# Performance work log

Hardware: AMD Instinct MI355X
Metric: run time of the kernel (lower is better)

The kernel has to match this reference:

```python
import jax, jax.numpy as jnp
import numpy as np

B, S, HID = 1, 2048, 2048
H, NOPE, ROPE, VDIM = 16, 128, 64, 128
QR, KVR = 1536, 512
IH, ID = 16, 128
TOPK = 512
THETA = 10000.0
EPS = 1e-6
SCALE = (NOPE + ROPE) ** -0.5
NEG = -1e9


def _cos_sin(s, dim, dtype):
    inv = 1.0 / (THETA ** (np.arange(0, dim, 2, dtype=np.float32) / dim))
    t = np.arange(s, dtype=np.float32)
    f = np.outer(t, inv)
    emb = np.concatenate([f, f], -1)
    return jnp.asarray(np.cos(emb), dtype), jnp.asarray(np.sin(emb), dtype)


def _rope(x, cos, sin):
    # x: [b,s,h,d]; cos/sin: [s,d]; NeoX-style rotate_half
    x1, x2 = jnp.split(x, 2, axis=-1)
    rot = jnp.concatenate([-x2, x1], axis=-1)
    return x * cos[None, :, None, :] + rot * sin[None, :, None, :]


def _rmsnorm(x, w):
    v = jnp.mean(x.astype(jnp.float32) ** 2, -1, keepdims=True)
    return (x.astype(jnp.float32) * jax.lax.rsqrt(v + EPS)).astype(x.dtype) * w


def _layernorm(x, w, b):
    m = jnp.mean(x, -1, keepdims=True)
    v = jnp.var(x, -1, keepdims=True)
    return (x - m) * jax.lax.rsqrt(v + EPS) * w + b


def setup_inputs() -> dict:
    key = jax.random.key(0)
    ks = jax.random.split(key, 12)
    g = lambda k, shp: jax.random.normal(k, shp, jnp.float32) * 0.02
    return {
        'hidden_states': jax.random.normal(ks[0], (B, S, HID), jnp.float32),
        'q_a_w': g(ks[1], (QR, HID)),
        'q_a_ln_w': jnp.ones((QR,), jnp.float32),
        'q_b_w': g(ks[2], (H * (NOPE + ROPE), QR)),
        'kv_a_w': g(ks[3], (KVR + ROPE, HID)),
        'kv_a_ln_w': jnp.ones((KVR,), jnp.float32),
        'kv_b_w': g(ks[4], (H * (NOPE + VDIM), KVR)),
        'o_w': g(ks[5], (HID, H * VDIM)),
        'idx_wq_b_w': g(ks[6], (IH * ID, QR)),
        'idx_wk_w': g(ks[7], (ID, HID)),
        'idx_kn_w': jnp.ones((ID,), jnp.float32),
        'idx_kn_b': jnp.zeros((ID,), jnp.float32),
        'idx_wproj_w': g(ks[8], (IH, HID)),
    }


def reference(hidden_states, q_a_w, q_a_ln_w, q_b_w, kv_a_w, kv_a_ln_w, kv_b_w, o_w,
              idx_wq_b_w, idx_wk_w, idx_kn_w, idx_kn_b, idx_wproj_w):
    b, s, _ = hidden_states.shape
    cos, sin = _cos_sin(s, ROPE, hidden_states.dtype)

    # --- MLA projections ---
    qr = _rmsnorm(hidden_states @ q_a_w.T, q_a_ln_w)                 # [b,s,QR]
    q = (qr @ q_b_w.T).reshape(b, s, H, NOPE + ROPE)
    q_nope, q_pe = q[..., :NOPE], q[..., NOPE:]
    q_pe = _rope(q_pe, cos, sin)
    ckv = hidden_states @ kv_a_w.T                                   # [b,s,KVR+ROPE]
    c_kv, k_pe = ckv[..., :KVR], ckv[..., KVR:]
    k_pe = _rope(k_pe[:, :, None, :], cos, sin)                      # [b,s,1,ROPE]
    kv = (_rmsnorm(c_kv, kv_a_ln_w) @ kv_b_w.T).reshape(b, s, H, NOPE + VDIM)
    k_nope, v = kv[..., :NOPE], kv[..., NOPE:]

    # --- DSA indexer: per-token importance scores ---
    iq = (qr @ idx_wq_b_w.T).reshape(b, s, IH, ID)
    iq = jnp.concatenate([_rope(iq[..., :ROPE], cos, sin), iq[..., ROPE:]], -1)
    ik = _layernorm(hidden_states @ idx_wk_w.T, idx_kn_w, idx_kn_b)  # [b,s,ID]
    ik_pe = _rope(ik[:, :, None, :ROPE], cos, sin)[:, :, 0, :]
    ik = jnp.concatenate([ik_pe, ik[..., ROPE:]], -1)
    iw = (hidden_states @ idx_wproj_w.T) * (IH ** -0.5)              # [b,s,IH]
    idx_scores = jnp.einsum('bqh,bhqk->bqk', iw,
                            jax.nn.relu(jnp.einsum('bqhd,bkd->bhqk', iq, ik)))
    causal = jnp.tril(jnp.ones((s, s), bool))
    idx_scores = jnp.where(causal[None], idx_scores, -jnp.inf)
    _, top_idx = jax.lax.top_k(idx_scores, TOPK)                     # [b,s,TOPK]
    bi = jnp.arange(b)[:, None, None]
    qi = jnp.arange(s)[None, :, None]
    keep = jnp.zeros((b, s, s), bool).at[bi, qi, top_idx].set(True)
    allowed = keep & causal[None]                                    # [b,s,s]

    # --- sparse top-k attention (top-k mask to -inf before softmax) ---
    qh = jnp.concatenate([q_nope, q_pe], -1)                         # [b,s,H,192]
    kh = jnp.concatenate([k_nope, jnp.broadcast_to(k_pe, (b, s, H, ROPE))], -1)
    scores = jnp.einsum('bqhd,bkhd->bhqk', qh, kh) * SCALE
    scores = jnp.where(allowed[:, None], scores, NEG)
    attn = jax.nn.softmax(scores, -1)
    out = jnp.einsum('bhqk,bkhd->bqhd', attn, v).reshape(b, s, H * VDIM)
    return out @ o_w.T
```

## Files before the change

kernel.cpp:

```cpp
#include <hip/hip_runtime.h>
#include <hip/hip_bf16.h>
#include <math.h>

#define SEQ 2048
#define HIDD 2048
#define QRANK 1536
#define KVRANK 512
#define TOPK 512
#define EPSF 1e-6f
#define SCALE_ATTN 0.07216878364870323f
#define NCAT 1680

typedef __attribute__((ext_vector_type(8))) short short8v;
typedef __attribute__((ext_vector_type(4))) short short4v;
typedef __attribute__((ext_vector_type(4))) float f32x4;

__device__ inline unsigned short f2bf(float f) {
    unsigned u = __float_as_uint(f);
    unsigned r = (u + 0x7FFFu + ((u >> 16) & 1u)) >> 16;
    return (unsigned short)r;
}
__device__ inline float bf2f(unsigned short b) {
    return __uint_as_float(((unsigned)b) << 16);
}
__device__ inline void split2(float x, unsigned short& h, unsigned short& l) {
    h = f2bf(x);
    l = f2bf(x - bf2f(h));
}

__device__ inline short4v ds_read_tr16(const void* p) {
#if __has_builtin(__builtin_amdgcn_ds_read_tr16_b64)
    return __builtin_amdgcn_ds_read_tr16_b64((short4v*)p);
#else
    const unsigned short* u = (const unsigned short*)p;
    short4v r;
    r[0] = (short)u[0]; r[1] = (short)u[16]; r[2] = (short)u[32]; r[3] = (short)u[48];
    return r;
#endif
}

__global__ __launch_bounds__(256) void cvt_bf16_4_kernel(
    const float* __restrict__ a, int na4, const float* __restrict__ b, int nb4,
    const float* __restrict__ c, int nc4, const float* __restrict__ d, int nd4,
    unsigned short* __restrict__ oa, unsigned short* __restrict__ ob,
    unsigned short* __restrict__ oc, unsigned short* __restrict__ od,
    float* __restrict__ cos_t, float* __restrict__ sin_t)
{
    if (blockIdx.x < SEQ && threadIdx.x < 32) {
        int s = blockIdx.x, i = threadIdx.x;
        double inv = pow(10000.0, -((double)(2 * i)) / 64.0);
        double f = (double)s * inv;
        cos_t[s * 32 + i] = (float)cos(f);
        sin_t[s * 32 + i] = (float)sin(f);
    }
    int total = na4 + nb4 + nc4 + nd4;
    for (int i = blockIdx.x * 256 + threadIdx.x; i < total; i += gridDim.x * 256) {
        const float* src; unsigned short* dst; int j = i;
        if (j < na4) { src = a; dst = oa; }
        else if ((j -= na4) < nb4) { src = b; dst = ob; }
        else if ((j -= nb4) < nc4) { src = c; dst = oc; }
        else { j -= nc4; src = d; dst = od; }
        float4 v = ((const float4*)src)[j];
        ushort4 o;
        o.x = f2bf(v.x); o.y = f2bf(v.y); o.z = f2bf(v.z); o.w = f2bf(v.w);
        ((ushort4*)dst)[j] = o;
    }
}

__global__ __launch_bounds__(256) void cvt_split3_kernel(
    const float* __restrict__ hidden, const float* __restrict__ q_a_w,
    const float* __restrict__ idx_wk_w, const float* __restrict__ idx_wproj_w,
    const float* __restrict__ wq,
    unsigned short* __restrict__ hidh, unsigned short* __restrict__ hidl,
    unsigned short* __restrict__ catwh, unsigned short* __restrict__ catwl,
    unsigned short* __restrict__ wqh, unsigned short* __restrict__ wql)
{
    const int nhid4 = HIDD * HIDD / 4;
    const int ncat4 = NCAT * HIDD / 4;
    const int nwq4  = HIDD * QRANK / 4;
    int total = nhid4 + ncat4 + nwq4;
    for (int i = blockIdx.x * 256 + threadIdx.x; i < total; i += gridDim.x * 256) {
        int j = i;
        const float4* s4;
        unsigned short *dh, *dl;
        float scale = 1.f;
        if (j < nhid4) {
            s4 = (const float4*)hidden + j; dh = hidh; dl = hidl;
        } else if ((j -= nhid4) < ncat4) {
            int row = (j * 4) >> 11;
            dh = catwh; dl = catwl;
            if (row < 1536) s4 = (const float4*)q_a_w + j;
            else if (row < 1664) s4 = (const float4*)idx_wk_w + (j - 1536 * 512);
            else { s4 = (const float4*)idx_wproj_w + (j - 1664 * 512); scale = 0.25f; }
        } else {
            j -= ncat4;
            s4 = (const float4*)wq + j; dh = wqh; dl = wql;
        }
        float4 v = *s4;
        float xs[4] = {v.x * scale, v.y * scale, v.z * scale, v.w * scale};
        ushort4 oh, ol;
        unsigned short h2, l2;
        split2(xs[0], h2, l2); oh.x = h2; ol.x = l2;
        split2(xs[1], h2, l2); oh.y = h2; ol.y = l2;
        split2(xs[2], h2, l2); oh.z = h2; ol.z = l2;
        split2(xs[3], h2, l2); oh.w = h2; ol.w = l2;
        ((ushort4*)dh)[j] = oh;
        ((ushort4*)dl)[j] = ol;
    }
}

__global__ __launch_bounds__(256) void wkt_kernel(const float* __restrict__ kvb,
                                                  unsigned short* __restrict__ wkt) {
    __shared__ float t[128][129];
    int h = blockIdx.x, n0 = blockIdx.y * 128;
    int tid = threadIdx.x;
    for (int it = tid; it < 128 * 32; it += 256) {
        int d = it >> 5, c4 = it & 31;
        float4 v = *(const float4*)(kvb + ((size_t)(h * 256 + d)) * 512 + n0 + c4 * 4);
        t[d][c4 * 4 + 0] = v.x; t[d][c4 * 4 + 1] = v.y;
        t[d][c4 * 4 + 2] = v.z; t[d][c4 * 4 + 3] = v.w;
    }
    __syncthreads();
    for (int it = tid; it < 128 * 32; it += 256) {
        int n = it >> 5, dc = it & 31;
        ushort4 o;
        o.x = f2bf(t[dc * 4 + 0][n]); o.y = f2bf(t[dc * 4 + 1][n]);
        o.z = f2bf(t[dc * 4 + 2][n]); o.w = f2bf(t[dc * 4 + 3][n]);
        *(ushort4*)(wkt + ((size_t)h * 512 + n0 + n) * 128 + dc * 4) = o;
    }
}

__global__ __launch_bounds__(256) void gemm_cat_split_kernel(
    const float* __restrict__ hidden, const float* __restrict__ q_a_w,
    const float* __restrict__ idx_wk_w, const float* __restrict__ idx_wproj_w,
    const unsigned short* __restrict__ hidh, const unsigned short* __restrict__ hidl,
    const unsigned short* __restrict__ catwh, const unsigned short* __restrict__ catwl,
    float* __restrict__ ccat)
{
    __shared__ __align__(16) unsigned short Ah[128 * 32], Al[128 * 32];
    __shared__ __align__(16) unsigned short Bh[128 * 32], Bl[128 * 32];
    int tid = threadIdx.x;
    int l = tid & 63, w = tid >> 6;
    int wr = w >> 1, wc = w & 1;
    int m0 = blockIdx.x * 128, n0 = blockIdx.y * 128;
    const bool pre = (hidh != nullptr);
    f32x4 acc[4][4] = {};
    for (int k0 = 0; k0 < HIDD; k0 += 32) {
        __syncthreads();
#pragma unroll
        for (int i = 0; i < 2; ++i) {
            int idx = tid + i * 256;
            int r = idx >> 2, cc = idx & 3;
            int sw = cc ^ (r & 3);
            int gb = n0 + r; if (gb > NCAT - 1) gb = NCAT - 1;
            if (pre) {
                size_t abase = (size_t)(m0 + r) * HIDD + k0 + cc * 8;
                *(short8v*)&Ah[r * 32 + sw * 8] = *(const short8v*)(hidh + abase);
                *(short8v*)&Al[r * 32 + sw * 8] = *(const short8v*)(hidl + abase);
                size_t bbase = (size_t)gb * HIDD + k0 + cc * 8;
                *(short8v*)&Bh[r * 32 + sw * 8] = *(const short8v*)(catwh + bbase);
                *(short8v*)&Bl[r * 32 + sw * 8] = *(const short8v*)(catwl + bbase);
            } else {
                {
                    const float* src = hidden + (size_t)(m0 + r) * HIDD + k0 + cc * 8;
                    float4 f0 = *(const float4*)src, f1 = *(const float4*)(src + 4);
                    float xs[8] = {f0.x, f0.y, f0.z, f0.w, f1.x, f1.y, f1.z, f1.w};
                    short8v dh, dl;
#pragma unroll
                    for (int e = 0; e < 8; ++e) {
                        unsigned short hh, ll; split2(xs[e], hh, ll);
                        dh[e] = (short)hh; dl[e] = (short)ll;
                    }
                    *(short8v*)&Ah[r * 32 + sw * 8] = dh;
                    *(short8v*)&Al[r * 32 + sw * 8] = dl;
                }
                {
                    float scale = 1.f;
                    const float* src;
                    if (gb < 1536) src = q_a_w + (size_t)gb * HIDD;
                    else if (gb < 1664) src = idx_wk_w + (size_t)(gb - 1536) * HIDD;
                    else { src = idx_wproj_w + (size_t)(gb - 1664) * HIDD; scale = 0.25f; }
                    src += k0 + cc * 8;
                    float4 f0 = *(const float4*)src, f1 = *(const float4*)(src + 4);
                    float xs[8] = {f0.x, f0.y, f0.z, f0.w, f1.x, f1.y, f1.z, f1.w};
                    short8v dh, dl;
#pragma unroll
                    for (int e = 0; e < 8; ++e) {
                        unsigned short hh, ll; split2(xs[e] * scale, hh, ll);
                        dh[e] = (short)hh; dl[e] = (short)ll;
                    }
                    *(short8v*)&Bh[r * 32 + sw * 8] = dh;
                    *(short8v*)&Bl[r * 32 + sw * 8] = dl;
                }
            }
        }
        __syncthreads();
        short8v avh[4], avl[4];
#pragma unroll
        for (int mt = 0; mt < 4; ++mt) {
            int row = wr * 64 + mt * 16 + (l & 15);
            int ch = (l >> 4) ^ (row & 3);
            avh[mt] = *(const short8v*)&Ah[row * 32 + ch * 8];
            avl[mt] = *(const short8v*)&Al[row * 32 + ch * 8];
        }
#pragma unroll
        for (int nt = 0; nt < 4; ++nt) {
            int row = wc * 64 + nt * 16 + (l & 15);
            int ch = (l >> 4) ^ (row & 3);
            short8v bvh = *(const short8v*)&Bh[row * 32 + ch * 8];
            short8v bvl = *(const short8v*)&Bl[row * 32 + ch * 8];
#pragma unroll
            for (int mt = 0; mt < 4; ++mt) {
                acc[mt][nt] = __builtin_amdgcn_mfma_f32_16x16x32_bf16(avh[mt], bvh, acc[mt][nt], 0, 0, 0);
                acc[mt][nt] = __builtin_amdgcn_mfma_f32_16x16x32_bf16(avh[mt], bvl, acc[mt][nt], 0, 0, 0);
                acc[mt][nt] = __builtin_amdgcn_mfma_f32_16x16x32_bf16(avl[mt], bvh, acc[mt][nt], 0, 0, 0);
            }
        }
    }
#pragma unroll
    for (int mt = 0; mt < 4; ++mt)
#pragma unroll
        for (int nt = 0; nt < 4; ++nt)
#pragma unroll
            for (int i = 0; i < 4; ++i) {
                int gm = m0 + wr * 64 + mt * 16 + (l >> 4) * 4 + i;
                int gn = n0 + wc * 64 + nt * 16 + (l & 15);
                if (gn < NCAT) ccat[(size_t)gm * NCAT + gn] = acc[mt][nt][i];
            }
}

__global__ __launch_bounds__(256) void gemm_iq_split_kernel(
    const float* __restrict__ qr, const float* __restrict__ wq,
    const unsigned short* __restrict__ qrh, const unsigned short* __restrict__ qrl,
    const unsigned short* __restrict__ wqh, const unsigned short* __restrict__ wql,
    const float* __restrict__ cos_t, const float* __restrict__ sin_t,
    unsigned short* __restrict__ iqh, unsigned short* __restrict__ iql)
{
    __shared__ __align__(16) unsigned short Ah[128 * 32], Al[128 * 32];
    __shared__ __align__(16) unsigned short Bh[128 * 32], Bl[128 * 32];
    int tid = threadIdx.x;
    int l = tid & 63, w = tid >> 6;
    int wr = w >> 1, wc = w & 1;
    int m0 = blockIdx.x * 128, n0 = blockIdx.y * 128;
    int hh_ = blockIdx.y;
    const bool pre = (wqh != nullptr);
    f32x4 acc[4][4] = {};
    for (int k0 = 0; k0 < QRANK; k0 += 32) {
        __syncthreads();
#pragma unroll
        for (int i = 0; i < 2; ++i) {
            int idx = tid + i * 256;
            int r = idx >> 2, cc = idx & 3;
            int sw = cc ^ (r & 3);
            if (pre) {
                size_t abase = (size_t)(m0 + r) * QRANK + k0 + cc * 8;
                *(short8v*)&Ah[r * 32 + sw * 8] = *(const short8v*)(qrh + abase);
                *(short8v*)&Al[r * 32 + sw * 8] = *(const short8v*)(qrl + abase);
                size_t bbase = (size_t)(n0 + r) * QRANK + k0 + cc * 8;
                *(short8v*)&Bh[r * 32 + sw * 8] = *(const short8v*)(wqh + bbase);
                *(short8v*)&Bl[r * 32 + sw * 8] = *(const short8v*)(wql + bbase);
            } else {
                {
                    const float* src = qr + (size_t)(m0 + r) * QRANK + k0 + cc * 8;
                    float4 f0 = *(const float4*)src, f1 = *(const float4*)(src + 4);
                    float xs[8] = {f0.x, f0.y, f0.z, f0.w, f1.x, f1.y, f1.z, f1.w};
                    short8v dh, dl;
#pragma unroll
                    for (int e = 0; e < 8; ++e) {
                        unsigned short h2, l2; split2(xs[e], h2, l2);
                        dh[e] = (short)h2; dl[e] = (short)l2;
                    }
                    *(short8v*)&Ah[r * 32 + sw * 8] = dh;
                    *(short8v*)&Al[r * 32 + sw * 8] = dl;
                }
                {
                    const float* src = wq + (size_t)(n0 + r) * QRANK + k0 + cc * 8;
                    float4 f0 = *(const float4*)src, f1 = *(const float4*)(src + 4);
                    float xs[8] = {f0.x, f0.y, f0.z, f0.w, f1.x, f1.y, f1.z, f1.w};
                    short8v dh, dl;
#pragma unroll
                    for (int e = 0; e < 8; ++e) {
                        unsigned short h2, l2; split2(xs[e], h2, l2);
                        dh[e] = (short)h2; dl[e] = (short)l2;
                    }
                    *(short8v*)&Bh[r * 32 + sw * 8] = dh;
                    *(short8v*)&Bl[r * 32 + sw * 8] = dl;
                }
            }
        }
        __syncthreads();
        short8v avh[4], avl[4];
#pragma unroll
        for (int mt = 0; mt < 4; ++mt) {
            int row = wr * 64 + mt * 16 + (l & 15);
            int ch = (l >> 4) ^ (row & 3);
            avh[mt] = *(const short8v*)&Ah[row * 32 + ch * 8];
            avl[mt] = *(const short8v*)&Al[row * 32 + ch * 8];
        }
#pragma unroll
        for (int nt = 0; nt < 4; ++nt) {
            int row = wc * 64 + nt * 16 + (l & 15);
            int ch = (l >> 4) ^ (row & 3);
            short8v bvh = *(const short8v*)&Bh[row * 32 + ch * 8];
            short8v bvl = *(const short8v*)&Bl[row * 32 + ch * 8];
#pragma unroll
            for (int mt = 0; mt < 4; ++mt) {
                acc[mt][nt] = __builtin_amdgcn_mfma_f32_16x16x32_bf16(avh[mt], bvh, acc[mt][nt], 0, 0, 0);
                acc[mt][nt] = __builtin_amdgcn_mfma_f32_16x16x32_bf16(avh[mt], bvl, acc[mt][nt], 0, 0, 0);
                acc[mt][nt] = __builtin_amdgcn_mfma_f32_16x16x32_bf16(avl[mt], bvh, acc[mt][nt], 0, 0, 0);
            }
        }
    }
    if (wc == 0) {
#pragma unroll
        for (int mt = 0; mt < 4; ++mt)
#pragma unroll
            for (int nt = 0; nt < 2; ++nt)
#pragma unroll
                for (int i = 0; i < 4; ++i) {
                    int q = m0 + wr * 64 + mt * 16 + (l >> 4) * 4 + i;
                    int dd = nt * 16 + (l & 15);
                    float c = cos_t[q * 32 + dd], s = sin_t[q * 32 + dd];
                    float x1 = acc[mt][nt][i], x2 = acc[mt][nt + 2][i];
                    acc[mt][nt][i] = x1 * c - x2 * s;
                    acc[mt][nt + 2][i] = x2 * c + x1 * s;
                }
    }
#pragma unroll
    for (int mt = 0; mt < 4; ++mt)
#pragma unroll
        for (int nt = 0; nt < 4; ++nt)
#pragma unroll
            for (int i = 0; i < 4; ++i) {
                int q = m0 + wr * 64 + mt * 16 + (l >> 4) * 4 + i;
                int d = wc * 64 + nt * 16 + (l & 15);
                size_t idx = ((size_t)q * 16 + hh_) * 128 + d;
                unsigned short h2, l2; split2(acc[mt][nt][i], h2, l2);
                iqh[idx] = h2; iql[idx] = l2;
            }
}

template <typename TA, typename TC>
__global__ __launch_bounds__(256) void mfma_nt_kernel(
    const TA* __restrict__ A, const unsigned short* __restrict__ B, TC* __restrict__ C,
    int M, int N, int K, int lda, int ldb, int ldc, long ab, long bb, long cb,
    const float* __restrict__ cos_t, const float* __restrict__ sin_t, int rope_mode)
{
    __shared__ __align__(16) unsigned short Asl[128 * 32];
    __shared__ __align__(16) unsigned short Bsl[128 * 32];
    int z = blockIdx.z;
    const TA* Az = A + (size_t)z * ab;
    const unsigned short* Bz = B + (size_t)z * bb;
    TC* Cz = C + (size_t)z * cb;
    int tid = threadIdx.x;
    int l = tid & 63, w = tid >> 6;
    int wr = w >> 1, wc = w & 1;
    int m0 = blockIdx.x * 128, n0 = blockIdx.y * 128;
    f32x4 acc[4][4] = {};

    for (int k0 = 0; k0 < K; k0 += 32) {
        __syncthreads();
#pragma unroll
        for (int i = 0; i < 2; ++i) {
            int idx = tid + i * 256;
            int r = idx >> 2, cc = idx & 3;
            int sw = cc ^ (r & 3);
            {
                short8v d;
                const TA* src = Az + (size_t)(m0 + r) * lda + k0 + cc * 8;
                if constexpr (sizeof(TA) == 2) {
                    d = *(const short8v*)src;
                } else {
                    float4 f0 = *(const float4*)src;
                    float4 f1 = *(const float4*)(src + 4);
                    d[0] = (short)f2bf(f0.x); d[1] = (short)f2bf(f0.y);
                    d[2] = (short)f2bf(f0.z); d[3] = (short)f2bf(f0.w);
                    d[4] = (short)f2bf(f1.x); d[5] = (short)f2bf(f1.y);
                    d[6] = (short)f2bf(f1.z); d[7] = (short)f2bf(f1.w);
                }
                *(short8v*)&Asl[r * 32 + sw * 8] = d;
            }
            {
                int gb = n0 + r; if (gb > N - 1) gb = N - 1;
                short8v d = *(const short8v*)(Bz + (size_t)gb * ldb + k0 + cc * 8);
                *(short8v*)&Bsl[r * 32 + sw * 8] = d;
            }
        }
        __syncthreads();
        short8v av[4], bv[4];
#pragma unroll
        for (int mt = 0; mt < 4; ++mt) {
            int row = wr * 64 + mt * 16 + (l & 15);
            int ch = (l >> 4) ^ (row & 3);
            av[mt] = *(const short8v*)&Asl[row * 32 + ch * 8];
        }
#pragma unroll
        for (int nt = 0; nt < 4; ++nt) {
            int row = wc * 64 + nt * 16 + (l & 15);
            int ch = (l >> 4) ^ (row & 3);
            bv[nt] = *(const short8v*)&Bsl[row * 32 + ch * 8];
        }
#pragma unroll
        for (int mt = 0; mt < 4; ++mt)
#pragma unroll
            for (int nt = 0; nt < 4; ++nt)
                acc[mt][nt] = __builtin_amdgcn_mfma_f32_16x16x32_bf16(av[mt], bv[nt], acc[mt][nt], 0, 0, 0);
    }
    if (rope_mode) {
        int gcol64 = (n0 >> 6) + wc;
        bool dorope = (rope_mode == 1) ? ((gcol64 % 3) == 2) : (gcol64 == 8);
        if (dorope) {
#pragma unroll
            for (int mt = 0; mt < 4; ++mt)
#pragma unroll
                for (int nt = 0; nt < 2; ++nt)
#pragma unroll
                    for (int i = 0; i < 4; ++i) {
                        int q = m0 + wr * 64 + mt * 16 + (l >> 4) * 4 + i;
                        int dd = nt * 16 + (l & 15);
                        float c = cos_t[q * 32 + dd], sn = sin_t[q * 32 + dd];
                        float x1 = acc[mt][nt][i], x2 = acc[mt][nt + 2][i];
                        acc[mt][nt][i] = x1 * c - x2 * sn;
                        acc[mt][nt + 2][i] = x2 * c + x1 * sn;
                    }
        }
    }
#pragma unroll
    for (int mt = 0; mt < 4; ++mt) {
#pragma unroll
        for (int nt = 0; nt < 4; ++nt) {
#pragma unroll
            for (int i = 0; i < 4; ++i) {
                int gm = m0 + wr * 64 + mt * 16 + (l >> 4) * 4 + i;
                int gn = n0 + wc * 64 + nt * 16 + (l & 15);
                if (gn < N) {
                    float v = acc[mt][nt][i];
                    if constexpr (sizeof(TC) == 4) Cz[(size_t)gm * ldc + gn] = v;
                    else Cz[(size_t)gm * ldc + gn] = f2bf(v);
                }
            }
        }
    }
}

__global__ __launch_bounds__(256) void rmsnorm_kernel(
    const float* __restrict__ in, const float* __restrict__ w, float* __restrict__ out,
    unsigned short* __restrict__ bf_out, unsigned short* __restrict__ bf_lo,
    int n, int in_stride)
{
    int row = blockIdx.x, tid = threadIdx.x;
    const float* x = in + (size_t)row * in_stride;
    float4 v[2];
    int cnt = 0;
    float ss = 0.f;
    int nf4 = n >> 2;
    for (int i = tid; i < nf4; i += 256) {
        float4 t = *(const float4*)(x + i * 4);
        v[cnt++] = t;
        ss += t.x * t.x + t.y * t.y + t.z * t.z + t.w * t.w;
    }
#pragma unroll
    for (int m = 32; m; m >>= 1) ss += __shfl_xor(ss, m);
    __shared__ float red[8];
    int wid = tid >> 6;
    if ((tid & 63) == 0) red[wid] = ss;
    __syncthreads();
    if (tid == 0) {
        float s = red[0] + red[1] + red[2] + red[3];
        red[4] = rsqrtf(s / (float)n + EPSF);
    }
    __syncthreads();
    float scale = red[4];
    cnt = 0;
    for (int i = tid; i < nf4; i += 256) {
        float4 t = v[cnt++];
        float4 wv = *(const float4*)(w + i * 4);
        float4 o;
        o.x = t.x * scale * wv.x; o.y = t.y * scale * wv.y;
        o.z = t.z * scale * wv.z; o.w = t.w * scale * wv.w;
        *(float4*)(out + (size_t)row * n + i * 4) = o;
        if (bf_out) {
            ushort4 ob;
            ob.x = f2bf(o.x); ob.y = f2bf(o.y); ob.z = f2bf(o.z); ob.w = f2bf(o.w);
            *(ushort4*)(bf_out + (size_t)row * n + i * 4) = ob;
            if (bf_lo) {
                ushort4 ol;
                ol.x = f2bf(o.x - bf2f(ob.x)); ol.y = f2bf(o.y - bf2f(ob.y));
                ol.z = f2bf(o.z - bf2f(ob.z)); ol.w = f2bf(o.w - bf2f(ob.w));
                *(ushort4*)(bf_lo + (size_t)row * n + i * 4) = ol;
            }
        }
    }
}

__global__ __launch_bounds__(256) void rmsnorm_khg_kernel(
    const float* __restrict__ ckv, const float* __restrict__ w,
    unsigned short* __restrict__ khg)
{
    int row = blockIdx.x, tid = threadIdx.x;
    const float* x = ckv + (size_t)row * 576;
    float4 v = make_float4(0.f, 0.f, 0.f, 0.f);
    float ss = 0.f;
    if (tid < 128) {
        v = *(const float4*)(x + tid * 4);
        ss = v.x * v.x + v.y * v.y + v.z * v.z + v.w * v.w;
    }
#pragma unroll
    for (int mm = 32; mm; mm >>= 1) ss += __shfl_xor(ss, mm);
    __shared__ float red[8];
    if ((tid & 63) == 0) red[tid >> 6] = ss;
    __syncthreads();
    if (tid == 0) red[4] = rsqrtf((red[0] + red[1] + red[2] + red[3]) * (1.f / 512.f) + EPSF);
    __syncthreads();
    float scale = red[4];
    if (tid < 128) {
        float4 wv = *(const float4*)(w + tid * 4);
        ushort4 ob;
        ob.x = f2bf(v.x * scale * wv.x); ob.y = f2bf(v.y * scale * wv.y);
        ob.z = f2bf(v.z * scale * wv.z); ob.w = f2bf(v.w * scale * wv.w);
        *(ushort4*)(khg + (size_t)row * 576 + tid * 4) = ob;
    } else if (tid < 192) {
        khg[(size_t)row * 576 + 512 + (tid - 128)] = f2bf(x[512 + tid - 128]);
    }
}

__global__ __launch_bounds__(64) void ln_rope_split_kernel(
    const float* __restrict__ in, int stride,
    const float* __restrict__ w, const float* __restrict__ b,
    const float* __restrict__ cos_t, const float* __restrict__ sin_t,
    unsigned short* __restrict__ ikh, unsigned short* __restrict__ ikl)
{
    int row = blockIdx.x, tid = threadIdx.x;
    const float* x = in + (size_t)row * stride;
    float x0 = x[tid], x1 = x[tid + 64];
    float s = x0 + x1, ss = x0 * x0 + x1 * x1;
#pragma unroll
    for (int m = 32; m; m >>= 1) { s += __shfl_xor(s, m); ss += __shfl_xor(ss, m); }
    float mean = s * (1.f / 128.f);
    float var = ss * (1.f / 128.f) - mean * mean;
    float r = rsqrtf(var + EPSF);
    float n0 = (x0 - mean) * r * w[tid] + b[tid];
    float n1 = (x1 - mean) * r * w[tid + 64] + b[tid + 64];
    float c = cos_t[row * 32 + (tid & 31)], sn = sin_t[row * 32 + (tid & 31)];
    float other = __shfl_xor(n0, 32);
    float r0 = (tid < 32) ? (n0 * c - other * sn) : (n0 * c + other * sn);
    unsigned short h2, l2;
    split2(r0, h2, l2);
    ikh[(size_t)row * 128 + tid] = h2; ikl[(size_t)row * 128 + tid] = l2;
    split2(n1, h2, l2);
    ikh[(size_t)row * 128 + 64 + tid] = h2; ikl[(size_t)row * 128 + 64 + tid] = l2;
}

__global__ __launch_bounds__(256) void idx_scores_mfma_kernel(
    const unsigned short* __restrict__ iqh, const unsigned short* __restrict__ iql,
    const unsigned short* __restrict__ ikh, const unsigned short* __restrict__ ikl,
    const float* __restrict__ iwsrc, int iw_stride,
    float* __restrict__ scores)
{
    int q0 = blockIdx.x * 64, k0 = blockIdx.y * 64;
    int tid = threadIdx.x;
    if (k0 > q0 + 63) {
        for (int t = tid; t < 64 * 64; t += 256) {
            int r = t >> 6, c = t & 63;
            scores[(size_t)(q0 + r) * SEQ + k0 + c] = -INFINITY;
        }
        return;
    }
    __shared__ __align__(16) unsigned short skh[64 * 128], skl[64 * 128];
    __shared__ __align__(16) unsigned short sqh[64 * 128], sql[64 * 128];
    __shared__ float iws[64][16];
    int l = tid & 63, w = tid >> 6;
    for (int it = tid; it < 64 * 16; it += 256) {
        int r = it >> 4, c = it & 15;
        int sw = c ^ (r & 15);
        *(short8v*)&skh[r * 128 + sw * 8] = *(const short8v*)(ikh + (size_t)(k0 + r) * 128 + c * 8);
        *(short8v*)&skl[r * 128 + sw * 8] = *(const short8v*)(ikl + (size_t)(k0 + r) * 128 + c * 8);
    }
    {
        int r = tid >> 2, c = tid & 3;
        *(float4*)&iws[r][c * 4] = *(const float4*)(iwsrc + (size_t)(q0 + r) * iw_stride + c * 4);
    }
    __syncthreads();
    short8v bhr[4][4], blr[4][4];
#pragma unroll
    for (int nt = 0; nt < 4; ++nt)
#pragma unroll
        for (int ks = 0; ks < 4; ++ks) {
            int brow = nt * 16 + (l & 15);
            int bch = ((l >> 4) + ks * 4) ^ (brow & 15);
            bhr[nt][ks] = *(const short8v*)&skh[brow * 128 + bch * 8];
            blr[nt][ks] = *(const short8v*)&skl[brow * 128 + bch * 8];
        }
    f32x4 acc[4] = {};
    for (int h = 0; h < 16; ++h) {
        __syncthreads();
        for (int it = tid; it < 64 * 16; it += 256) {
            int r = it >> 4, c = it & 15;
            int sw = c ^ (r & 15);
            size_t base = ((size_t)(q0 + r) * 16 + h) * 128 + c * 8;
            *(short8v*)&sqh[r * 128 + sw * 8] = *(const short8v*)(iqh + base);
            *(short8v*)&sql[r * 128 + sw * 8] = *(const short8v*)(iql + base);
        }
        __syncthreads();
        f32x4 dot[4] = {};
#pragma unroll
        for (int ks = 0; ks < 4; ++ks) {
            int arow = w * 16 + (l & 15);
            int ach = ((l >> 4) + ks * 4) ^ (arow & 15);
            short8v ah = *(const short8v*)&sqh[arow * 128 + ach * 8];
            short8v al = *(const short8v*)&sql[arow * 128 + ach * 8];
#pragma unroll
            for (int nt = 0; nt < 4; ++nt) {
                dot[nt] = __builtin_amdgcn_mfma_f32_16x16x32_bf16(ah, bhr[nt][ks], dot[nt], 0, 0, 0);
                dot[nt] = __builtin_amdgcn_mfma_f32_16x16x32_bf16(ah, blr[nt][ks], dot[nt], 0, 0, 0);
                dot[nt] = __builtin_amdgcn_mfma_f32_16x16x32_bf16(al, bhr[nt][ks], dot[nt], 0, 0, 0);
            }
        }
#pragma unroll
        for (int nt = 0; nt < 4; ++nt)
#pragma unroll
            for (int i = 0; i < 4; ++i) {
                float wv = iws[w * 16 + (l >> 4) * 4 + i][h];
                acc[nt][i] += wv * fmaxf(dot[nt][i], 0.f);
            }
    }
#pragma unroll
    for (int nt = 0; nt < 4; ++nt)
#pragma unroll
        for (int i = 0; i < 4; ++i) {
            int q = q0 + w * 16 + (l >> 4) * 4 + i;
            int k = k0 + nt * 16 + (l & 15);
            scores[(size_t)q * SEQ + k] = (k <= q) ? acc[nt][i] : -INFINITY;
        }
}

__global__ __launch_bounds__(1024) void topk_kernel(
    const float* __restrict__ scores, int* __restrict__ sel)
{
    int qi = blockIdx.x, tid = threadIdx.x;
    __shared__ unsigned long long keys[2048];
    const float* srow = scores + (size_t)qi * SEQ;
#pragma unroll
    for (int r = 0; r < 2; ++r) {
        int k = tid + r * 1024;
        unsigned u = __float_as_uint(srow[k]);
        unsigned mv = (u & 0x80000000u) ? ~u : (u | 0x80000000u);
        keys[k] = ((unsigned long long)mv << 32) | (unsigned)(2047 - k);
    }
    for (int ksz = 2; ksz <= 2048; ksz <<= 1) {
        for (int j = ksz >> 1; j > 0; j >>= 1) {
            __syncthreads();
#pragma unroll 1
            for (int r = 0; r < 2; ++r) {
                int i = tid + r * 1024;
                int ixj = i ^ j;
                if (ixj > i) {
                    unsigned long long a = keys[i], b = keys[ixj];
                    bool dir = ((i & ksz) == 0);
                    if ((a < b) == dir) { keys[i] = b; keys[ixj] = a; }
                }
            }
        }
    }
    __syncthreads();
    if (tid < TOPK) {
        int k = 2047 - (int)(keys[tid] & 0xFFFFFFFFu);
        sel[(size_t)qi * TOPK + tid] = (tid <= qi) ? k : -1;
    }
}

__global__ __launch_bounds__(256) void attn_mfma_kernel(
    const unsigned short* __restrict__ qabs,
    const float* __restrict__ qsrc,
    const unsigned short* __restrict__ khg,
    const int* __restrict__ sel,
    unsigned short* __restrict__ ocomp)
{
    __shared__ __align__(16) char smem[77312];
    unsigned short* plds = (unsigned short*)(smem + 74752);
    float* smax = (float*)(smem + 76800);
    float* ssum = (float*)(smem + 77056);

    const int qi = blockIdx.x;
    const int tid = threadIdx.x;
    const int l = tid & 63, w = tid >> 6;
    const int lg = l >> 4, lr = l & 15;
    const int nv = min(TOPK, qi + 1);
    const int ntile = (nv + 63) >> 6;
    const int krow = w * 16 + lr;

    const int ck = tid >> 6, cc = tid & 63;
    const int pk = tid >> 3, pc = tid & 7;
    const int* selrow = sel + (size_t)qi * TOPK;

    short8v aq[18];
    {
        const unsigned short* qa = qabs + ((size_t)qi * 16 + lr) * 512 + lg * 8;
#pragma unroll
        for (int ks = 0; ks < 16; ++ks)
            aq[ks] = *(const short8v*)(qa + ks * 32);
        const float* qp = qsrc + (size_t)qi * 3072 + lr * 192 + 128 + lg * 8;
#pragma unroll
        for (int ks = 0; ks < 2; ++ks) {
            float4 f0 = *(const float4*)(qp + ks * 32);
            float4 f1 = *(const float4*)(qp + ks * 32 + 4);
            short8v d;
            d[0] = (short)f2bf(f0.x); d[1] = (short)f2bf(f0.y);
            d[2] = (short)f2bf(f0.z); d[3] = (short)f2bf(f0.w);
            d[4] = (short)f2bf(f1.x); d[5] = (short)f2bf(f1.y);
            d[6] = (short)f2bf(f1.z); d[7] = (short)f2bf(f1.w);
            aq[16 + ks] = d;
        }
    }

    const int sbase = krow * 32 + (lg >> 1) * 2080 + (lg & 1) * 16;
    const int vboff = w * 16640 + lg * 256 + lr * 2;

    float m[4] = {-1e30f, -1e30f, -1e30f, -1e30f};
    float lsum[4] = {0.f, 0.f, 0.f, 0.f};
    f32x4 oacc[8] = {};

    for (int t = 0; t < ntile; ++t) {
        const int j0 = t * 64;
        __syncthreads();
#pragma unroll
        for (int j = 0; j < 16; ++j) {
            int sv = selrow[j0 + ck + 4 * j];
            if (sv < 0) sv = 0;
            short8v v = *(const short8v*)(khg + (size_t)sv * 576 + cc * 8);
            *(short8v*)(smem + (cc >> 1) * 2080 + (ck + 4 * j) * 32 + (cc & 1) * 16) = v;
        }
#pragma unroll
        for (int j = 0; j < 2; ++j) {
            int sv = selrow[j0 + pk + 32 * j];
            if (sv < 0) sv = 0;
            short8v v = *(const short8v*)(khg + (size_t)sv * 576 + 512 + pc * 8);
            int key = pk + 32 * j;
            *(short8v*)(smem + 66560 + ((key * 128 + pc * 16) ^ ((key & 7) << 4))) = v;
        }
        __syncthreads();
        f32x4 s = {};
#pragma unroll
        for (int ks = 0; ks < 16; ++ks) {
            short8v b = *(const short8v*)(smem + sbase + ks * 4160);
            s = __builtin_amdgcn_mfma_f32_16x16x32_bf16(aq[ks], b, s, 0, 0, 0);
        }
#pragma unroll
        for (int ks = 0; ks < 2; ++ks) {
            short8v b = *(const short8v*)(smem + 66560 +
                ((krow * 128 + ks * 64 + lg * 16) ^ ((krow & 7) << 4)));
            s = __builtin_amdgcn_mfma_f32_16x16x32_bf16(aq[16 + ks], b, s, 0, 0, 0);
        }
        bool kvalid = (j0 + krow) < nv;
#pragma unroll
        for (int i = 0; i < 4; ++i)
            s[i] = kvalid ? s[i] * SCALE_ATTN : -1e30f;
        float tm[4];
#pragma unroll
        for (int i = 0; i < 4; ++i) tm[i] = s[i];
#pragma unroll
        for (int sh = 1; sh < 16; sh <<= 1)
#pragma unroll
            for (int i = 0; i < 4; ++i) tm[i] = fmaxf(tm[i], __shfl_xor(tm[i], sh));
        if (lr == 0) *(float4*)&smax[w * 16 + lg * 4] = make_float4(tm[0], tm[1], tm[2], tm[3]);
        __syncthreads();
        float mn[4], scl[4];
#pragma unroll
        for (int i = 0; i < 4; ++i) {
            int h = lg * 4 + i;
            float tmax = fmaxf(fmaxf(smax[h], smax[16 + h]), fmaxf(smax[32 + h], smax[48 + h]));
            mn[i] = fmaxf(m[i], tmax);
            scl[i] = __expf(m[i] - mn[i]);
            m[i] = mn[i];
        }
        float p[4], rs[4];
#pragma unroll
        for (int i = 0; i < 4; ++i) { p[i] = __expf(s[i] - mn[i]); rs[i] = p[i]; }
#pragma unroll
        for (int sh = 1; sh < 16; sh <<= 1)
#pragma unroll
            for (int i = 0; i < 4; ++i) rs[i] += __shfl_xor(rs[i], sh);
        if (lr == 0) *(float4*)&ssum[w * 16 + lg * 4] = make_float4(rs[0], rs[1], rs[2], rs[3]);
        {
            ushort4 pb;
            pb.x = f2bf(p[0]); pb.y = f2bf(p[1]); pb.z = f2bf(p[2]); pb.w = f2bf(p[3]);
            *(ushort4*)&plds[(w * 16 + lr) * 16 + lg * 4] = pb;
        }
        __syncthreads();
#pragma unroll
        for (int i = 0; i < 4; ++i) {
            int h = lg * 4 + i;
            float ts = ssum[h] + ssum[16 + h] + ssum[32 + h] + ssum[48 + h];
            lsum[i] = lsum[i] * scl[i] + ts;
        }
#pragma unroll
        for (int nt = 0; nt < 8; ++nt)
#pragma unroll
            for (int i = 0; i < 4; ++i) oacc[nt][i] *= scl[i];
#pragma unroll
        for (int kb = 0; kb < 2; ++kb) {
            short8v af;
#pragma unroll
            for (int j = 0; j < 8; ++j)
                af[j] = (short)plds[(kb * 32 + lg * 8 + j) * 16 + lr];
#pragma unroll
            for (int nt = 0; nt < 8; ++nt) {
                const char* a = smem + vboff + kb * 1024 + nt * 2080;
                short4v t0 = ds_read_tr16(a);
                short4v t1 = ds_read_tr16(a + 128);
                short8v bf = __builtin_shufflevector(t0, t1, 0, 1, 2, 3, 4, 5, 6, 7);
                oacc[nt] = __builtin_amdgcn_mfma_f32_16x16x32_bf16(af, bf, oacc[nt], 0, 0, 0);
            }
        }
    }
    float inv[4];
#pragma unroll
    for (int i = 0; i < 4; ++i) inv[i] = 1.f / lsum[i];
    unsigned short* ob = ocomp + (size_t)qi * 16 * 512;
#pragma unroll
    for (int nt = 0; nt < 8; ++nt) {
        int d = w * 128 + nt * 16 + lr;
#pragma unroll
        for (int i = 0; i < 4; ++i) {
            int h = lg * 4 + i;
            ob[h * 512 + d] = f2bf(oacc[nt][i] * inv[i]);
        }
    }
}

extern "C" void kernel_launch(void* const* d_in, const int* in_sizes, int n_in,
                              void* d_out, int out_size, void* d_ws, size_t ws_size,
                              hipStream_t stream) {
    (void)in_sizes; (void)n_in; (void)out_size;
    const float* hidden      = (const float*)d_in[0];
    const float* q_a_w       = (const float*)d_in[1];
    const float* q_a_ln_w    = (const float*)d_in[2];
    const float* q_b_w       = (const float*)d_in[3];
    const float* kv_a_w      = (const float*)d_in[4];
    const float* kv_a_ln_w   = (const float*)d_in[5];
    const float* kv_b_w      = (const float*)d_in[6];
    const float* o_w         = (const float*)d_in[7];
    const float* idx_wq_b_w  = (const float*)d_in[8];
    const float* idx_wk_w    = (const float*)d_in[9];
    const float* idx_kn_w    = (const float*)d_in[10];
    const float* idx_kn_b    = (const float*)d_in[11];
    const float* idx_wproj_w = (const float*)d_in[12];
    float* out = (float*)d_out;

    char* ws = (char*)d_ws;
    size_t off = 0;
    auto alloc = [&](size_t nbytes) -> void* {
        void* p = ws + off;
        off = (off + nbytes + 255) & ~(size_t)255;
        return p;
    };
    float* cos_t = (float*)alloc((size_t)SEQ * 32 * 4);
    float* sin_t = (float*)alloc((size_t)SEQ * 32 * 4);
    float* qbuf  = (float*)alloc((size_t)SEQ * 3072 * 4);
    float* ckv   = (float*)alloc((size_t)SEQ * 576 * 4);
    int*   sel   = (int*)alloc((size_t)SEQ * TOPK * 4);
    unsigned short* khg      = (unsigned short*)alloc((size_t)SEQ * 576 * 2);
    unsigned short* attno_bf = (unsigned short*)alloc((size_t)SEQ * 2048 * 2);
    unsigned short* qr_bf    = (unsigned short*)alloc((size_t)SEQ * QRANK * 2);
    unsigned short* q_b_bf   = (unsigned short*)alloc((size_t)3072 * QRANK * 2);
    unsigned short* kv_a_bf  = (unsigned short*)alloc((size_t)576 * HIDD * 2);
    unsigned short* o_w_bf   = (unsigned short*)alloc((size_t)HIDD * 2048 * 2);
    unsigned short* kv_b_bf  = (unsigned short*)alloc((size_t)4096 * 512 * 2);
    unsigned short* wkt      = (unsigned short*)alloc((size_t)16 * 512 * 128 * 2);
    size_t mark = off;
    float* qr    = (float*)alloc((size_t)SEQ * QRANK * 4);
    float* ccat  = (float*)alloc((size_t)SEQ * NCAT * 4);
    float* scores = (float*)alloc((size_t)SEQ * SEQ * 4);
    unsigned short* iqh = (unsigned short*)alloc((size_t)SEQ * 2048 * 2);
    unsigned short* iql = (unsigned short*)alloc((size_t)SEQ * 2048 * 2);
    unsigned short* ikh = (unsigned short*)alloc((size_t)SEQ * 128 * 2);
    unsigned short* ikl = (unsigned short*)alloc((size_t)SEQ * 128 * 2);
    unsigned short* hidh  = (unsigned short*)alloc((size_t)HIDD * HIDD * 2);
    unsigned short* hidl  = (unsigned short*)alloc((size_t)HIDD * HIDD * 2);
    unsigned short* catwh = (unsigned short*)alloc((size_t)NCAT * HIDD * 2);
    unsigned short* catwl = (unsigned short*)alloc((size_t)NCAT * HIDD * 2);
    unsigned short* wqh   = (unsigned short*)alloc((size_t)HIDD * QRANK * 2);
    unsigned short* wql   = (unsigned short*)alloc((size_t)HIDD * QRANK * 2);
    unsigned short* qr_l  = (unsigned short*)alloc((size_t)SEQ * QRANK * 2);
    bool fast = (off <= ws_size);
    if (!fast) {
        hidh = hidl = catwh = catwl = wqh = wql = qr_l = nullptr;
    }
    off = mark;
    unsigned short* qabsb = (unsigned short*)alloc((size_t)SEQ * 16 * 512 * 2);
    unsigned short* ocomp = (unsigned short*)alloc((size_t)SEQ * 16 * 512 * 2);

    cvt_bf16_4_kernel<<<2048, 256, 0, stream>>>(
        q_b_w, 3072 * QRANK / 4, kv_a_w, 576 * HIDD / 4,
        o_w, HIDD * 2048 / 4, kv_b_w, 4096 * 512 / 4,
        q_b_bf, kv_a_bf, o_w_bf, kv_b_bf, cos_t, sin_t);
    wkt_kernel<<<dim3(16, 4), 256, 0, stream>>>(kv_b_w, wkt);
    if (fast)
        cvt_split3_kernel<<<2048, 256, 0, stream>>>(
            hidden, q_a_w, idx_wk_w, idx_wproj_w, idx_wq_b_w,
            hidh, hidl, catwh, catwl, wqh, wql);

    gemm_cat_split_kernel<<<dim3(16, 14), 256, 0, stream>>>(
        hidden, q_a_w, idx_wk_w, idx_wproj_w, hidh, hidl, catwh, catwl, ccat);

    rmsnorm_kernel<<<SEQ, 256, 0, stream>>>(ccat, q_a_ln_w, qr, qr_bf, qr_l, QRANK, NCAT);

    ln_rope_split_kernel<<<SEQ, 64, 0, stream>>>(ccat + 1536, NCAT, idx_kn_w, idx_kn_b, cos_t, sin_t, ikh, ikl);

    mfma_nt_kernel<unsigned short, float><<<dim3(16, 24, 1), 256, 0, stream>>>(
        qr_bf, q_b_bf, qbuf, SEQ, 3072, QRANK, QRANK, QRANK, 3072, 0L, 0L, 0L,
        cos_t, sin_t, 1);

    mfma_nt_kernel<float, float><<<dim3(16, 5, 1), 256, 0, stream>>>(
        hidden, kv_a_bf, ckv, SEQ, 576, HIDD, HIDD, HIDD, 576, 0L, 0L, 0L,
        cos_t, sin_t, 2);
    rmsnorm_khg_kernel<<<SEQ, 256, 0, stream>>>(ckv, kv_a_ln_w, khg);

    gemm_iq_split_kernel<<<dim3(16, 16), 256, 0, stream>>>(
        qr, idx_wq_b_w, qr_bf, qr_l, wqh, wql, cos_t, sin_t, iqh, iql);

    idx_scores_mfma_kernel<<<dim3(32, 32), 256, 0, stream>>>(iqh, iql, ikh, ikl, ccat + 1664, NCAT, scores);
    topk_kernel<<<SEQ, 1024, 0, stream>>>(scores, sel);

    mfma_nt_kernel<float, unsigned short><<<dim3(16, 4, 16), 256, 0, stream>>>(
        qbuf, wkt, qabsb, SEQ, 512, 128, 3072, 128, 16 * 512,
        192L, 512L * 128L, 512L, nullptr, nullptr, 0);

    attn_mfma_kernel<<<SEQ, 256, 0, stream>>>(qabsb, qbuf, khg, sel, ocomp);

    mfma_nt_kernel<unsigned short, unsigned short><<<dim3(16, 1, 16), 256, 0, stream>>>(
        ocomp, kv_b_bf + (size_t)128 * 512, attno_bf, SEQ, 128, 512,
        16 * 512, 512, 2048, 512L, 256L * 512L, 128L, nullptr, nullptr, 0);

    mfma_nt_kernel<unsigned short, float><<<dim3(16, 16, 1), 256, 0, stream>>>(
        attno_bf, o_w_bf, out, SEQ, HIDD, 2048, 2048, 2048, HIDD, 0L, 0L, 0L,
        nullptr, nullptr, 0);
}
```

Baseline: 802.8 us.

## Fuse norm kernels, emit bf16 q_nope, drop LDS staging in indexer, tweak attention

```diff
diff --git a/kernel.cpp b/kernel.cpp
--- a/kernel.cpp
+++ b/kernel.cpp
@@ -344,7 +344,8 @@
 __global__ __launch_bounds__(256) void mfma_nt_kernel(
     const TA* __restrict__ A, const unsigned short* __restrict__ B, TC* __restrict__ C,
     int M, int N, int K, int lda, int ldb, int ldc, long ab, long bb, long cb,
-    const float* __restrict__ cos_t, const float* __restrict__ sin_t, int rope_mode)
+    const float* __restrict__ cos_t, const float* __restrict__ sin_t, int rope_mode,
+    unsigned short* __restrict__ qnope)
 {
     __shared__ __align__(16) unsigned short Asl[128 * 32];
     __shared__ __align__(16) unsigned short Bsl[128 * 32];
@@ -437,59 +438,88 @@
                     float v = acc[mt][nt][i];
                     if constexpr (sizeof(TC) == 4) Cz[(size_t)gm * ldc + gn] = v;
                     else Cz[(size_t)gm * ldc + gn] = f2bf(v);
+                    if (rope_mode == 1 && qnope) {
+                        int gh = gn / 192, gr = gn - gh * 192;
+                        if (gr < 128)
+                            qnope[(size_t)gm * 2048 + gh * 128 + gr] = f2bf(v);
+                    }
                 }
             }
         }
     }
 }
 
-__global__ __launch_bounds__(256) void rmsnorm_kernel(
-    const float* __restrict__ in, const float* __restrict__ w, float* __restrict__ out,
-    unsigned short* __restrict__ bf_out, unsigned short* __restrict__ bf_lo,
-    int n, int in_stride)
+__global__ __launch_bounds__(256) void norms_fused_kernel(
+    const float* __restrict__ ccat,
+    const float* __restrict__ q_a_ln_w, float* __restrict__ qr_out,
+    unsigned short* __restrict__ qr_bf, unsigned short* __restrict__ qr_lo,
+    const float* __restrict__ ikn_w, const float* __restrict__ ikn_b,
+    const float* __restrict__ cos_t, const float* __restrict__ sin_t,
+    unsigned short* __restrict__ ikh, unsigned short* __restrict__ ikl)
 {
-    int row = blockIdx.x, tid = threadIdx.x;
-    const float* x = in + (size_t)row * in_stride;
-    float4 v[2];
-    int cnt = 0;
-    float ss = 0.f;
-    int nf4 = n >> 2;
-    for (int i = tid; i < nf4; i += 256) {
-        float4 t = *(const float4*)(x + i * 4);
-        v[cnt++] = t;
-        ss += t.x * t.x + t.y * t.y + t.z * t.z + t.w * t.w;
-    }
-#pragma unroll
-    for (int m = 32; m; m >>= 1) ss += __shfl_xor(ss, m);
-    __shared__ float red[8];
-    int wid = tid >> 6;
-    if ((tid & 63) == 0) red[wid] = ss;
-    __syncthreads();
-    if (tid == 0) {
-        float s = red[0] + red[1] + red[2] + red[3];
-        red[4] = rsqrtf(s / (float)n + EPSF);
-    }
-    __syncthreads();
-    float scale = red[4];
-    cnt = 0;
-    for (int i = tid; i < nf4; i += 256) {
-        float4 t = v[cnt++];
-        float4 wv = *(const float4*)(w + i * 4);
-        float4 o;
-        o.x = t.x * scale * wv.x; o.y = t.y * scale * wv.y;
-        o.z = t.z * scale * wv.z; o.w = t.w * scale * wv.w;
-        *(float4*)(out + (size_t)row * n + i * 4) = o;
-        if (bf_out) {
+    int blk = blockIdx.x, tid = threadIdx.x;
+    if (blk < SEQ) {
+        int row = blk;
+        const float* x = ccat + (size_t)row * NCAT;
+        float4 v[2];
+        int cnt = 0;
+        float ss = 0.f;
+        const int nf4 = QRANK >> 2;
+        for (int i = tid; i < nf4; i += 256) {
+            float4 t = *(const float4*)(x + i * 4);
+            v[cnt++] = t;
+            ss += t.x * t.x + t.y * t.y + t.z * t.z + t.w * t.w;
+        }
+#pragma unroll
+        for (int m = 32; m; m >>= 1) ss += __shfl_xor(ss, m);
+        __shared__ float red[8];
+        if ((tid & 63) == 0) red[tid >> 6] = ss;
+        __syncthreads();
+        if (tid == 0) {
+            float s = red[0] + red[1] + red[2] + red[3];
+            red[4] = rsqrtf(s / (float)QRANK + EPSF);
+        }
+        __syncthreads();
+        float scale = red[4];
+        cnt = 0;
+        for (int i = tid; i < nf4; i += 256) {
+            float4 t = v[cnt++];
+            float4 wv = *(const float4*)(q_a_ln_w + i * 4);
+            float4 o;
+            o.x = t.x * scale * wv.x; o.y = t.y * scale * wv.y;
+            o.z = t.z * scale * wv.z; o.w = t.w * scale * wv.w;
+            *(float4*)(qr_out + (size_t)row * QRANK + i * 4) = o;
             ushort4 ob;
             ob.x = f2bf(o.x); ob.y = f2bf(o.y); ob.z = f2bf(o.z); ob.w = f2bf(o.w);
-            *(ushort4*)(bf_out + (size_t)row * n + i * 4) = ob;
-            if (bf_lo) {
+            *(ushort4*)(qr_bf + (size_t)row * QRANK + i * 4) = ob;
+            if (qr_lo) {
                 ushort4 ol;
                 ol.x = f2bf(o.x - bf2f(ob.x)); ol.y = f2bf(o.y - bf2f(ob.y));
                 ol.z = f2bf(o.z - bf2f(ob.z)); ol.w = f2bf(o.w - bf2f(ob.w));
-                *(ushort4*)(bf_lo + (size_t)row * n + i * 4) = ol;
-            }
-        }
+                *(ushort4*)(qr_lo + (size_t)row * QRANK + i * 4) = ol;
+            }
+        }
+    } else {
+        if (tid >= 64) return;
+        int row = blk - SEQ;
+        const float* x = ccat + (size_t)row * NCAT + 1536;
+        float x0 = x[tid], x1 = x[tid + 64];
+        float s = x0 + x1, ss = x0 * x0 + x1 * x1;
+#pragma unroll
+        for (int m = 32; m; m >>= 1) { s += __shfl_xor(s, m); ss += __shfl_xor(ss, m); }
+        float mean = s * (1.f / 128.f);
+        float var = ss * (1.f / 128.f) - mean * mean;
+        float r = rsqrtf(var + EPSF);
+        float n0 = (x0 - mean) * r * ikn_w[tid] + ikn_b[tid];
+        float n1 = (x1 - mean) * r * ikn_w[tid + 64] + ikn_b[tid + 64];
+        float c = cos_t[row * 32 + (tid & 31)], sn = sin_t[row * 32 + (tid & 31)];
+        float other = __shfl_xor(n0, 32);
+        float r0 = (tid < 32) ? (n0 * c - other * sn) : (n0 * c + other * sn);
+        unsigned short h2, l2;
+        split2(r0, h2, l2);
+        ikh[(size_t)row * 128 + tid] = h2; ikl[(size_t)row * 128 + tid] = l2;
+        split2(n1, h2, l2);
+        ikh[(size_t)row * 128 + 64 + tid] = h2; ikl[(size_t)row * 128 + 64 + tid] = l2;
     }
 }
 
@@ -524,33 +554,6 @@
     }
 }
 
-__global__ __launch_bounds__(64) void ln_rope_split_kernel(
-    const float* __restrict__ in, int stride,
-    const float* __restrict__ w, const float* __restrict__ b,
-    const float* __restrict__ cos_t, const float* __restrict__ sin_t,
-    unsigned short* __restrict__ ikh, unsigned short* __restrict__ ikl)
-{
-    int row = blockIdx.x, tid = threadIdx.x;
-    const float* x = in + (size_t)row * stride;
-    float x0 = x[tid], x1 = x[tid + 64];
-    float s = x0 + x1, ss = x0 * x0 + x1 * x1;
-#pragma unroll
-    for (int m = 32; m; m >>= 1) { s += __shfl_xor(s, m); ss += __shfl_xor(ss, m); }
-    float mean = s * (1.f / 128.f);
-    float var = ss * (1.f / 128.f) - mean * mean;
-    float r = rsqrtf(var + EPSF);
-    float n0 = (x0 - mean) * r * w[tid] + b[tid];
-    float n1 = (x1 - mean) * r * w[tid + 64] + b[tid + 64];
-    float c = cos_t[row * 32 + (tid & 31)], sn = sin_t[row * 32 + (tid & 31)];
-    float other = __shfl_xor(n0, 32);
-    float r0 = (tid < 32) ? (n0 * c - other * sn) : (n0 * c + other * sn);
-    unsigned short h2, l2;
-    split2(r0, h2, l2);
-    ikh[(size_t)row * 128 + tid] = h2; ikl[(size_t)row * 128 + tid] = l2;
-    split2(n1, h2, l2);
-    ikh[(size_t)row * 128 + 64 + tid] = h2; ikl[(size_t)row * 128 + 64 + tid] = l2;
-}
-
 __global__ __launch_bounds__(256) void idx_scores_mfma_kernel(
     const unsigned short* __restrict__ iqh, const unsigned short* __restrict__ iql,
     const unsigned short* __restrict__ ikh, const unsigned short* __restrict__ ikl,
@@ -566,16 +569,8 @@
         }
         return;
     }
-    __shared__ __align__(16) unsigned short skh[64 * 128], skl[64 * 128];
-    __shared__ __align__(16) unsigned short sqh[64 * 128], sql[64 * 128];
     __shared__ float iws[64][16];
     int l = tid & 63, w = tid >> 6;
-    for (int it = tid; it < 64 * 16; it += 256) {
-        int r = it >> 4, c = it & 15;
-        int sw = c ^ (r & 15);
-        *(short8v*)&skh[r * 128 + sw * 8] = *(const short8v*)(ikh + (size_t)(k0 + r) * 128 + c * 8);
-        *(short8v*)&skl[r * 128 + sw * 8] = *(const short8v*)(ikl + (size_t)(k0 + r) * 128 + c * 8);
-    }
     {
         int r = tid >> 2, c = tid & 3;
         *(float4*)&iws[r][c * 4] = *(const float4*)(iwsrc + (size_t)(q0 + r) * iw_stride + c * 4);
@@ -586,29 +581,19 @@
     for (int nt = 0; nt < 4; ++nt)
 #pragma unroll
         for (int ks = 0; ks < 4; ++ks) {
-            int brow = nt * 16 + (l & 15);
-            int bch = ((l >> 4) + ks * 4) ^ (brow & 15);
-            bhr[nt][ks] = *(const short8v*)&skh[brow * 128 + bch * 8];
-            blr[nt][ks] = *(const short8v*)&skl[brow * 128 + bch * 8];
+            size_t base = (size_t)(k0 + nt * 16 + (l & 15)) * 128 + ks * 32 + (l >> 4) * 8;
+            bhr[nt][ks] = *(const short8v*)(ikh + base);
+            blr[nt][ks] = *(const short8v*)(ikl + base);
         }
     f32x4 acc[4] = {};
+    const int arow = q0 + w * 16 + (l & 15);
     for (int h = 0; h < 16; ++h) {
-        __syncthreads();
-        for (int it = tid; it < 64 * 16; it += 256) {
-            int r = it >> 4, c = it & 15;
-            int sw = c ^ (r & 15);
-            size_t base = ((size_t)(q0 + r) * 16 + h) * 128 + c * 8;
-            *(short8v*)&sqh[r * 128 + sw * 8] = *(const short8v*)(iqh + base);
-            *(short8v*)&sql[r * 128 + sw * 8] = *(const short8v*)(iql + base);
-        }
-        __syncthreads();
         f32x4 dot[4] = {};
 #pragma unroll
         for (int ks = 0; ks < 4; ++ks) {
-            int arow = w * 16 + (l & 15);
-            int ach = ((l >> 4) + ks * 4) ^ (arow & 15);
-            short8v ah = *(const short8v*)&sqh[arow * 128 + ach * 8];
-            short8v al = *(const short8v*)&sql[arow * 128 + ach * 8];
+            size_t abase = ((size_t)arow * 16 + h) * 128 + ks * 32 + (l >> 4) * 8;
+            short8v ah = *(const short8v*)(iqh + abase);
+            short8v al = *(const short8v*)(iql + abase);
 #pragma unroll
             for (int nt = 0; nt < 4; ++nt) {
                 dot[nt] = __builtin_amdgcn_mfma_f32_16x16x32_bf16(ah, bhr[nt][ks], dot[nt], 0, 0, 0);
@@ -676,10 +661,10 @@
     const int* __restrict__ sel,
     unsigned short* __restrict__ ocomp)
 {
-    __shared__ __align__(16) char smem[77312];
+    __shared__ __align__(16) char smem[77824];
     unsigned short* plds = (unsigned short*)(smem + 74752);
-    float* smax = (float*)(smem + 76800);
-    float* ssum = (float*)(smem + 77056);
+    float* smax = (float*)(smem + 77312);
+    float* ssum = (float*)(smem + 77568);
 
     const int qi = blockIdx.x;
     const int tid = threadIdx.x;
@@ -740,6 +725,7 @@
         }
         __syncthreads();
         f32x4 s = {};
+        __builtin_amdgcn_s_setprio(1);
 #pragma unroll
         for (int ks = 0; ks < 16; ++ks) {
             short8v b = *(const short8v*)(smem + sbase + ks * 4160);
@@ -751,6 +737,7 @@
                 ((krow * 128 + ks * 64 + lg * 16) ^ ((krow & 7) << 4)));
             s = __builtin_amdgcn_mfma_f32_16x16x32_bf16(aq[16 + ks], b, s, 0, 0, 0);
         }
+        __builtin_amdgcn_s_setprio(0);
         bool kvalid = (j0 + krow) < nv;
 #pragma unroll
         for (int i = 0; i < 4; ++i)
@@ -781,11 +768,9 @@
 #pragma unroll
             for (int i = 0; i < 4; ++i) rs[i] += __shfl_xor(rs[i], sh);
         if (lr == 0) *(float4*)&ssum[w * 16 + lg * 4] = make_float4(rs[0], rs[1], rs[2], rs[3]);
-        {
-            ushort4 pb;
-            pb.x = f2bf(p[0]); pb.y = f2bf(p[1]); pb.z = f2bf(p[2]); pb.w = f2bf(p[3]);
-            *(ushort4*)&plds[(w * 16 + lr) * 16 + lg * 4] = pb;
-        }
+#pragma unroll
+        for (int i = 0; i < 4; ++i)
+            plds[(lg * 4 + i) * 80 + krow] = f2bf(p[i]);
         __syncthreads();
 #pragma unroll
         for (int i = 0; i < 4; ++i) {
@@ -797,12 +782,10 @@
         for (int nt = 0; nt < 8; ++nt)
 #pragma unroll
             for (int i = 0; i < 4; ++i) oacc[nt][i] *= scl[i];
+        __builtin_amdgcn_s_setprio(1);
 #pragma unroll
         for (int kb = 0; kb < 2; ++kb) {
-            short8v af;
-#pragma unroll
-            for (int j = 0; j < 8; ++j)
-                af[j] = (short)plds[(kb * 32 + lg * 8 + j) * 16 + lr];
+            short8v af = *(const short8v*)&plds[lr * 80 + kb * 32 + lg * 8];
 #pragma unroll
             for (int nt = 0; nt < 8; ++nt) {
                 const char* a = smem + vboff + kb * 1024 + nt * 2080;
@@ -812,6 +795,7 @@
                 oacc[nt] = __builtin_amdgcn_mfma_f32_16x16x32_bf16(af, bf, oacc[nt], 0, 0, 0);
             }
         }
+        __builtin_amdgcn_s_setprio(0);
     }
     float inv[4];
 #pragma unroll
@@ -867,6 +851,7 @@
     unsigned short* o_w_bf   = (unsigned short*)alloc((size_t)HIDD * 2048 * 2);
     unsigned short* kv_b_bf  = (unsigned short*)alloc((size_t)4096 * 512 * 2);
     unsigned short* wkt      = (unsigned short*)alloc((size_t)16 * 512 * 128 * 2);
+    unsigned short* qnope_bf = attno_bf;
     size_t mark = off;
     float* qr    = (float*)alloc((size_t)SEQ * QRANK * 4);
     float* ccat  = (float*)alloc((size_t)SEQ * NCAT * 4);
@@ -903,17 +888,16 @@
     gemm_cat_split_kernel<<<dim3(16, 14), 256, 0, stream>>>(
         hidden, q_a_w, idx_wk_w, idx_wproj_w, hidh, hidl, catwh, catwl, ccat);
 
-    rmsnorm_kernel<<<SEQ, 256, 0, stream>>>(ccat, q_a_ln_w, qr, qr_bf, qr_l, QRANK, NCAT);
-
-    ln_rope_split_kernel<<<SEQ, 64, 0, stream>>>(ccat + 1536, NCAT, idx_kn_w, idx_kn_b, cos_t, sin_t, ikh, ikl);
+    norms_fused_kernel<<<2 * SEQ, 256, 0, stream>>>(
+        ccat, q_a_ln_w, qr, qr_bf, qr_l, idx_kn_w, idx_kn_b, cos_t, sin_t, ikh, ikl);
 
     mfma_nt_kernel<unsigned short, float><<<dim3(16, 24, 1), 256, 0, stream>>>(
         qr_bf, q_b_bf, qbuf, SEQ, 3072, QRANK, QRANK, QRANK, 3072, 0L, 0L, 0L,
-        cos_t, sin_t, 1);
+        cos_t, sin_t, 1, qnope_bf);
 
     mfma_nt_kernel<float, float><<<dim3(16, 5, 1), 256, 0, stream>>>(
         hidden, kv_a_bf, ckv, SEQ, 576, HIDD, HIDD, HIDD, 576, 0L, 0L, 0L,
-        cos_t, sin_t, 2);
+        cos_t, sin_t, 2, nullptr);
     rmsnorm_khg_kernel<<<SEQ, 256, 0, stream>>>(ckv, kv_a_ln_w, khg);
 
     gemm_iq_split_kernel<<<dim3(16, 16), 256, 0, stream>>>(
@@ -922,17 +906,17 @@
     idx_scores_mfma_kernel<<<dim3(32, 32), 256, 0, stream>>>(iqh, iql, ikh, ikl, ccat + 1664, NCAT, scores);
     topk_kernel<<<SEQ, 1024, 0, stream>>>(scores, sel);
 
-    mfma_nt_kernel<float, unsigned short><<<dim3(16, 4, 16), 256, 0, stream>>>(
-        qbuf, wkt, qabsb, SEQ, 512, 128, 3072, 128, 16 * 512,
-        192L, 512L * 128L, 512L, nullptr, nullptr, 0);
+    mfma_nt_kernel<unsigned short, unsigned short><<<dim3(16, 4, 16), 256, 0, stream>>>(
+        qnope_bf, wkt, qabsb, SEQ, 512, 128, 2048, 128, 16 * 512,
+        128L, 512L * 128L, 512L, nullptr, nullptr, 0, nullptr);
 
     attn_mfma_kernel<<<SEQ, 256, 0, stream>>>(qabsb, qbuf, khg, sel, ocomp);
 
     mfma_nt_kernel<unsigned short, unsigned short><<<dim3(16, 1, 16), 256, 0, stream>>>(
         ocomp, kv_b_bf + (size_t)128 * 512, attno_bf, SEQ, 128, 512,
-        16 * 512, 512, 2048, 512L, 256L * 512L, 128L, nullptr, nullptr, 0);
+        16 * 512, 512, 2048, 512L, 256L * 512L, 128L, nullptr, nullptr, 0, nullptr);
 
     mfma_nt_kernel<unsigned short, float><<<dim3(16, 16, 1), 256, 0, stream>>>(
         attno_bf, o_w_bf, out, SEQ, HIDD, 2048, 2048, 2048, HIDD, 0L, 0L, 0L,
-        nullptr, nullptr, 0);
-}
+        nullptr, nullptr, 0, nullptr);
+}
```

Measured after the change: 801.9 us. About the same (-0.1%).
